# Optimization experiments

Hardware: AMD Instinct MI355X
Metric: run time of the kernel (lower is better)

The kernel has to match this reference:

```python
import jax, jax.numpy as jnp
import numpy as np

N_NODES = 32768
EMB_DIM = 128
N_CODES = 4096
N_GRAPHS = 512
ALPHA = 0.5            # args.alpha_init buffer
COMMIT_W = 1.0         # args.commitment_weight
BN_EPS = 1e-5


def setup_inputs() -> dict:
    key = jax.random.key(0)
    ks = jax.random.split(key, 8)
    node_feat = jax.random.normal(ks[0], (N_NODES, EMB_DIM), dtype=jnp.float32)
    score = jax.random.uniform(ks[1], (N_NODES, 1), dtype=jnp.float32)
    batch = jnp.sort(jax.random.randint(ks[2], (N_NODES,), 0, N_GRAPHS)).astype(jnp.int64)
    codebook_c = jax.random.normal(ks[3], (N_CODES, EMB_DIM), dtype=jnp.float32)
    codebook_s = jax.random.normal(ks[4], (N_CODES, EMB_DIM), dtype=jnp.float32)
    w1 = jax.random.normal(ks[5], (EMB_DIM, 2 * EMB_DIM), dtype=jnp.float32) * (1.0 / np.sqrt(EMB_DIM))
    b1 = jnp.zeros((2 * EMB_DIM,), dtype=jnp.float32)
    gamma = jnp.ones((2 * EMB_DIM,), dtype=jnp.float32)
    beta = jnp.zeros((2 * EMB_DIM,), dtype=jnp.float32)
    run_mean = jnp.zeros((2 * EMB_DIM,), dtype=jnp.float32)
    run_var = jnp.ones((2 * EMB_DIM,), dtype=jnp.float32)
    w2 = jax.random.normal(ks[6], (2 * EMB_DIM, 1), dtype=jnp.float32) * (1.0 / np.sqrt(2 * EMB_DIM))
    b2 = jnp.zeros((1,), dtype=jnp.float32)
    return {"node_feat": node_feat, "score": score, "batch": batch,
            "codebook_c": codebook_c, "codebook_s": codebook_s,
            "w1": w1, "b1": b1, "gamma": gamma, "beta": beta,
            "run_mean": run_mean, "run_var": run_var, "w2": w2, "b2": b2}


def _vector_quantize(x, codebook):
    # squared euclidean distance [N, K]; argmin lookup with straight-through.
    d2 = (jnp.sum(x * x, axis=-1, keepdims=True)
          - 2.0 * (x @ codebook.T)
          + jnp.sum(codebook * codebook, axis=-1))
    idx = jnp.argmin(d2, axis=-1)                     # [N]
    quantize = codebook[idx]                          # gather [N, D]
    commit_loss = jnp.mean((jax.lax.stop_gradient(quantize) - x) ** 2) * COMMIT_W
    out = x + jax.lax.stop_gradient(quantize - x)     # straight-through estimator
    return out, idx, commit_loss


def _mean_pool(x, batch):
    sums = jax.ops.segment_sum(x, batch, num_segments=N_GRAPHS)
    counts = jax.ops.segment_sum(jnp.ones((x.shape[0], 1), x.dtype), batch, num_segments=N_GRAPHS)
    return sums / jnp.maximum(counts, 1.0)


def reference(node_feat, score, batch, codebook_c, codebook_s,
              w1, b1, gamma, beta, run_mean, run_var, w2, b2):
    h_c = node_feat * score + ALPHA * node_feat * (1.0 - score)
    h_s = node_feat * (1.0 - score) + ALPHA * node_feat * score
    vq_c, _, cmt_loss_c = _vector_quantize(h_c, codebook_c)
    vq_s, _, cmt_loss_s = _vector_quantize(h_s, codebook_s)
    c_node_feat = node_feat * score + vq_c
    s_node_feat = node_feat * (1.0 - score) + vq_s
    c_graph_feat = _mean_pool(c_node_feat, batch)
    s_graph_feat = _mean_pool(s_node_feat, batch)
    # classifier: Linear -> BatchNorm1d (eval) -> ReLU -> Dropout(identity) -> Linear
    h = c_graph_feat @ w1 + b1
    h = (h - run_mean) * jax.lax.rsqrt(run_var + BN_EPS) * gamma + beta
    h = jax.nn.relu(h)
    c_logit = h @ w2 + b2
    return (c_logit, c_graph_feat, s_graph_feat, cmt_loss_c, cmt_loss_s, c_node_feat, s_node_feat)
```

## Files before the change

### kernel.cpp

```cpp
#include <hip/hip_runtime.h>
#include <hip/hip_bf16.h>

#define NODES   32768
#define DIM     128
#define NCODES  4096
#define NGRAPHS 512

#define OFF_LOGIT 0
#define OFF_CG    512
#define OFF_SG    66048
#define OFF_LC    131584
#define OFF_LS    131585
#define OFF_CN    131586
#define OFF_SN    4325890

#define SPLIT_U16   263680
#define PLANE_U16   524288
#define SLOT_F32    1180416

#define WS_CNORM    0
#define WS_IDX      32768
#define WS_LOSS     294912
#define WS_FLAGCNT  294928
#define WS_STARTS   294936
#define WS_FLAGLIST 296988
#define FLAG_CAP    32767

typedef __attribute__((ext_vector_type(8))) short bf16x8_t;
typedef __attribute__((ext_vector_type(4))) float f32x4_t;

__device__ __forceinline__ float h_of(float x, float sc, int cb) {
    float omsc = __fsub_rn(1.0f, sc);
    float half_x = __fmul_rn(0.5f, x);
    if (cb == 0)
        return __fadd_rn(__fmul_rn(x, sc), __fmul_rn(half_x, omsc));
    else
        return __fadd_rn(__fmul_rn(x, omsc), __fmul_rn(half_x, sc));
}

__device__ __forceinline__ unsigned short f2bf(float f) {
    __hip_bfloat16 b = __float2bfloat16(f);
    return *reinterpret_cast<unsigned short*>(&b);
}
__device__ __forceinline__ float bf2f(unsigned short u) {
    __hip_bfloat16 b = *reinterpret_cast<__hip_bfloat16*>(&u);
    return __bfloat162float(b);
}

__device__ __forceinline__ void gload_lds16(const void* g, void* l) {
    __builtin_amdgcn_global_load_lds(
        (const __attribute__((address_space(1))) int*)g,
        (__attribute__((address_space(3))) int*)l, 16, 0, 0);
}

__global__ __launch_bounds__(256) void prep_kernel(
    const float* __restrict__ cb_c, const float* __restrict__ cb_s,
    const int* __restrict__ batch,
    float* __restrict__ cnorm, unsigned short* __restrict__ splits,
    int* __restrict__ starts, int* __restrict__ flagcnt)
{
    int gwave = (blockIdx.x * 256 + threadIdx.x) >> 6;
    int lane  = threadIdx.x & 63;

    if (gwave < 2 * NCODES) {
        int cb = gwave >> 12, row = gwave & (NCODES - 1);
        const float* cp = (cb ? cb_s : cb_c) + (size_t)row * DIM;
        float2 v = ((const float2*)cp)[lane];
        float p = __fadd_rn(__fmul_rn(v.x, v.x), __fmul_rn(v.y, v.y));
        #pragma unroll
        for (int off = 32; off; off >>= 1) p = __fadd_rn(p, __shfl_xor(p, off, 64));
        if (lane == 0) cnorm[cb * NCODES + row] = p;
        unsigned short h0 = f2bf(v.x), h1 = f2bf(v.y);
        unsigned short l0 = f2bf(__fsub_rn(v.x, bf2f(h0)));
        unsigned short l1 = f2bf(__fsub_rn(v.y, bf2f(h1)));
        unsigned int* hp = (unsigned int*)(splits + (size_t)(cb * 2 + 0) * PLANE_U16);
        unsigned int* lp = (unsigned int*)(splits + (size_t)(cb * 2 + 1) * PLANE_U16);
        hp[row * 64 + lane] = (unsigned int)h0 | ((unsigned int)h1 << 16);
        lp[row * 64 + lane] = (unsigned int)l0 | ((unsigned int)l1 << 16);
    } else {
        int w1 = gwave - 2 * NCODES;
        int g = w1 * 64 + lane;
        if (g <= NGRAPHS) {
            int lo = 0, hi = NODES;
            while (lo < hi) { int mid = (lo + hi) >> 1; if (batch[mid] < g) lo = mid + 1; else hi = mid; }
            starts[g] = lo;
        }
        if (w1 == 0 && lane < 2) flagcnt[lane] = 0;
    }
}

__global__ __launch_bounds__(256, 2) void vq_main_kernel(
    const float* __restrict__ node_feat, const float* __restrict__ score,
    const unsigned short* __restrict__ splits, const float* __restrict__ cnorm,
    int* __restrict__ idx_ws, int* __restrict__ flagcnt, int* __restrict__ flaglist,
    unsigned long long* __restrict__ slots)
{
    __shared__ unsigned short lds[32768];
    const int cb    = blockIdx.y;
    const int nbase = blockIdx.x * 128;
    const int tid = threadIdx.x;
    const int w   = tid >> 6;
    const int l15 = tid & 15;
    const int lg  = (tid & 63) >> 4;
    const int swz = (tid & 7) << 4;
    const float* cnp = cnorm + cb * NCODES;

    if (tid < 128) slots[(size_t)cb * NODES + nbase + tid] = ~0ull;

    #pragma unroll
    for (int i = 0; i < 16; ++i) {
        int idx = i * 1024 + tid * 4;
        int row = idx >> 7, k = idx & 127;
        float4 x = *(const float4*)&node_feat[(size_t)(nbase + row) * DIM + k];
        float sc = score[nbase + row];
        float h0 = h_of(x.x, sc, cb), h1 = h_of(x.y, sc, cb);
        float h2 = h_of(x.z, sc, cb), h3 = h_of(x.w, sc, cb);
        unsigned short u0 = f2bf(h0), u1 = f2bf(h1), u2 = f2bf(h2), u3 = f2bf(h3);
        unsigned short v0 = f2bf(__fsub_rn(h0, bf2f(u0))), v1 = f2bf(__fsub_rn(h1, bf2f(u1)));
        unsigned short v2 = f2bf(__fsub_rn(h2, bf2f(u2))), v3 = f2bf(__fsub_rn(h3, bf2f(u3)));
        int abyte = row * 256 + ((2 * k) ^ ((row & 7) << 4));
        uint2 hw; hw.x = (unsigned)u0 | ((unsigned)u1 << 16); hw.y = (unsigned)u2 | ((unsigned)u3 << 16);
        uint2 lw; lw.x = (unsigned)v0 | ((unsigned)v1 << 16); lw.y = (unsigned)v2 | ((unsigned)v3 << 16);
        *(uint2*)((char*)lds + abyte) = hw;
        *(uint2*)((char*)lds + 32768 + abyte) = lw;
    }
    __syncthreads();

    bf16x8_t ahi[2][4], alo[2][4];
    int colbyte[4];
    #pragma unroll
    for (int ch = 0; ch < 4; ++ch) colbyte[ch] = (ch * 64 + lg * 16) ^ swz;
    #pragma unroll
    for (int rs = 0; rs < 2; ++rs)
        #pragma unroll
        for (int ch = 0; ch < 4; ++ch) {
            int row = 32 * w + 16 * rs + l15;
            int off = row * 256 + colbyte[ch];
            ahi[rs][ch] = *(const bf16x8_t*)((const char*)lds + off);
            alo[rs][ch] = *(const bf16x8_t*)((const char*)lds + 32768 + off);
        }
    __syncthreads();

    const unsigned short* wplane = splits + (size_t)(cb * 2 + (w >> 1)) * PLANE_U16;
    int soff[8];
    #pragma unroll
    for (int i = 0; i < 8; ++i) {
        int row = ((w & 1) << 5) + i * 4 + lg;
        soff[i] = row * 256 + ((l15 * 16) ^ ((row & 7) << 4));
    }

    {
        const char* tb = (const char*)wplane;
        #pragma unroll
        for (int i = 0; i < 8; ++i)
            gload_lds16(tb + soff[i], (char*)lds + w * 8192 + i * 1024);
    }
    float cnc[4], cnn[4];
    #pragma unroll
    for (int cs = 0; cs < 4; ++cs) cnc[cs] = cnp[cs * 16 + l15];
    __syncthreads();

    const float NEG_INF = -3.4e38f;
    float b1v[2][4], b2v[2][4]; int b1i[2][4];
    #pragma unroll
    for (int rs = 0; rs < 2; ++rs)
        #pragma unroll
        for (int r = 0; r < 4; ++r) { b1v[rs][r] = NEG_INF; b2v[rs][r] = NEG_INF; b1i[rs][r] = 0; }

    for (int t = 0; t < 64; ++t) {
        int bs_cur = (t & 1) << 15;
        if (t < 63) {
            int bs_nxt = ((t + 1) & 1) << 15;
            const char* tb = (const char*)wplane + (t + 1) * 16384;
            #pragma unroll
            for (int i = 0; i < 8; ++i)
                gload_lds16(tb + soff[i], (char*)lds + bs_nxt + w * 8192 + i * 1024);
            #pragma unroll
            for (int cs = 0; cs < 4; ++cs) cnn[cs] = cnp[(t + 1) * 64 + cs * 16 + l15];
        }

        f32x4_t acc[2][4];
        #pragma unroll
        for (int cs = 0; cs < 4; ++cs) {
            float iv = -0.5f * cnc[cs];
            f32x4_t ini = {iv, iv, iv, iv};
            acc[0][cs] = ini; acc[1][cs] = ini;
        }

        #pragma unroll
        for (int ch = 0; ch < 4; ++ch) {
            #pragma unroll
            for (int cs = 0; cs < 4; ++cs) {
                const char* bp = (const char*)lds + bs_cur + (cs * 16 + l15) * 256 + colbyte[ch];
                bf16x8_t bhi = *(const bf16x8_t*)bp;
                bf16x8_t blo = *(const bf16x8_t*)(bp + 16384);
                #pragma unroll
                for (int rs = 0; rs < 2; ++rs) {
                    acc[rs][cs] = __builtin_amdgcn_mfma_f32_16x16x32_bf16(ahi[rs][ch], bhi, acc[rs][cs], 0, 0, 0);
                    acc[rs][cs] = __builtin_amdgcn_mfma_f32_16x16x32_bf16(alo[rs][ch], bhi, acc[rs][cs], 0, 0, 0);
                    acc[rs][cs] = __builtin_amdgcn_mfma_f32_16x16x32_bf16(ahi[rs][ch], blo, acc[rs][cs], 0, 0, 0);
                }
            }
        }

        #pragma unroll
        for (int cs = 0; cs < 4; ++cs) {
            int code = t * 64 + cs * 16 + l15;
            #pragma unroll
            for (int rs = 0; rs < 2; ++rs)
                #pragma unroll
                for (int r = 0; r < 4; ++r) {
                    float a = acc[rs][cs][r];
                    bool gt = a > b1v[rs][r];
                    float nb2 = __builtin_amdgcn_fmed3f(a, b1v[rs][r], b2v[rs][r]);
                    if (gt) b1i[rs][r] = code;
                    b1v[rs][r] = fmaxf(a, b1v[rs][r]);
                    b2v[rs][r] = nb2;
                }
        }
        #pragma unroll
        for (int cs = 0; cs < 4; ++cs) cnc[cs] = cnn[cs];
        __syncthreads();
    }

    #pragma unroll
    for (int off = 1; off < 16; off <<= 1) {
        #pragma unroll
        for (int rs = 0; rs < 2; ++rs)
            #pragma unroll
            for (int r = 0; r < 4; ++r) {
                float ov1 = __shfl_xor(b1v[rs][r], off, 64);
                int   oi  = __shfl_xor(b1i[rs][r], off, 64);
                float ov2 = __shfl_xor(b2v[rs][r], off, 64);
                bool take = (ov1 > b1v[rs][r]) || (ov1 == b1v[rs][r] && oi < b1i[rs][r]);
                float loser = fminf(ov1, b1v[rs][r]);
                b1v[rs][r] = fmaxf(ov1, b1v[rs][r]);
                if (take) b1i[rs][r] = oi;
                b2v[rs][r] = fmaxf(loser, fmaxf(ov2, b2v[rs][r]));
            }
    }
    if (l15 == 0) {
        #pragma unroll
        for (int rs = 0; rs < 2; ++rs)
            #pragma unroll
            for (int r = 0; r < 4; ++r) {
                int node = nbase + 32 * w + 16 * rs + 4 * lg + r;
                idx_ws[cb * NODES + node] = b1i[rs][r];
                if (b1v[rs][r] - b2v[rs][r] < 0.04f) {
                    int p = atomicAdd(flagcnt + cb, 1);
                    if (p < FLAG_CAP) flaglist[cb * FLAG_CAP + p] = node;
                }
            }
    }
}

__global__ __launch_bounds__(256) void vq_cleanup_kernel(
    const float* __restrict__ node_feat, const float* __restrict__ score,
    const float* __restrict__ cb_c, const float* __restrict__ cb_s,
    const float* __restrict__ cnorm, const int* __restrict__ flagcnt,
    const int* __restrict__ flaglist, unsigned long long* __restrict__ slots)
{
    __shared__ float cbT[128][65];
    __shared__ float hbuf[4][128];
    const int cb  = blockIdx.y;
    const int seg = blockIdx.x & 63;
    const int ng  = blockIdx.x >> 6;
    const float* cbp = cb ? cb_s : cb_c;
    const int* list = flaglist + cb * FLAG_CAP;
    int cnt = flagcnt[cb]; if (cnt > FLAG_CAP) cnt = FLAG_CAP;
    const int tid = threadIdx.x, w = tid >> 6, l = tid & 63;

    {
        int c = tid >> 2, ks = (tid & 3) * 32;
        const float* src = cbp + (size_t)(seg * 64 + c) * DIM + ks;
        #pragma unroll
        for (int j = 0; j < 8; ++j) {
            float4 v = *(const float4*)(src + j * 4);
            cbT[ks + j * 4 + 0][c] = v.x;
            cbT[ks + j * 4 + 1][c] = v.y;
            cbT[ks + j * 4 + 2][c] = v.z;
            cbT[ks + j * 4 + 3][c] = v.w;
        }
    }
    const int mycode = seg * 64 + l;
    const float cn = cnorm[cb * NCODES + mycode];
    __syncthreads();

    for (int base = ng * 4; base < cnt; base += 32) {
        int e = base + w;
        bool valid = e < cnt;
        int node = list[valid ? e : 0];
        float sc = score[node];
        float x0 = node_feat[(size_t)node * DIM + l];
        float x1 = node_feat[(size_t)node * DIM + 64 + l];
        float h0 = h_of(x0, sc, cb), h1 = h_of(x1, sc, cb);
        hbuf[w][l] = h0; hbuf[w][64 + l] = h1;
        float sxx = __fadd_rn(__fmul_rn(h0, h0), __fmul_rn(h1, h1));
        #pragma unroll
        for (int off = 32; off; off >>= 1) sxx = __fadd_rn(sxx, __shfl_xor(sxx, off, 64));
        asm volatile("s_waitcnt lgkmcnt(0)" ::: "memory");

        float p0 = 0.f, p1 = 0.f, p2 = 0.f, p3 = 0.f;
        #pragma unroll 8
        for (int m = 0; m < 32; ++m) {
            p0 = fmaf(hbuf[w][4 * m + 0], cbT[4 * m + 0][l], p0);
            p1 = fmaf(hbuf[w][4 * m + 1], cbT[4 * m + 1][l], p1);
            p2 = fmaf(hbuf[w][4 * m + 2], cbT[4 * m + 2][l], p2);
            p3 = fmaf(hbuf[w][4 * m + 3], cbT[4 * m + 3][l], p3);
        }
        float dot = __fadd_rn(__fadd_rn(p0, p1), __fadd_rn(p2, p3));
        float d2 = __fadd_rn(__fsub_rn(sxx, __fmul_rn(2.0f, dot)), cn);

        unsigned b = __float_as_uint(d2);
        unsigned key = (b & 0x80000000u) ? ~b : (b | 0x80000000u);
        unsigned long long pk = ((unsigned long long)key << 32) | (unsigned)mycode;
        #pragma unroll
        for (int off = 1; off < 64; off <<= 1) {
            unsigned long long o = __shfl_xor(pk, off, 64);
            pk = (o < pk) ? o : pk;
        }
        if (valid && l == 0)
            atomicMin(&slots[(size_t)cb * NODES + node], pk);
        asm volatile("s_waitcnt lgkmcnt(0)" ::: "memory");
    }
}

__global__ __launch_bounds__(256) void flag_writeback_kernel(
    const int* __restrict__ flagcnt, const int* __restrict__ flaglist,
    const unsigned long long* __restrict__ slots, int* __restrict__ idx_ws)
{
    int gt = blockIdx.x * 256 + threadIdx.x;
    int c0 = flagcnt[0]; if (c0 > FLAG_CAP) c0 = FLAG_CAP;
    int c1 = flagcnt[1]; if (c1 > FLAG_CAP) c1 = FLAG_CAP;
    for (int e = gt; e < 2 * FLAG_CAP; e += 256 * 256) {
        int cb = (e >= FLAG_CAP) ? 1 : 0;
        int i = e - cb * FLAG_CAP;
        int cnt = cb ? c1 : c0;
        if (i < cnt) {
            int node = flaglist[cb * FLAG_CAP + i];
            idx_ws[cb * NODES + node] =
                (int)(slots[(size_t)cb * NODES + node] & 0xFFFFFFFFull);
        }
    }
}

__global__ __launch_bounds__(256) void gather_kernel(
    const float* __restrict__ node_feat, const float* __restrict__ score,
    const float* __restrict__ cb_c, const float* __restrict__ cb_s,
    const int* __restrict__ idx_all, float* __restrict__ out,
    double* __restrict__ partials)
{
    __shared__ float redc[4], reds[4];
    int wave = threadIdx.x >> 6, lane = threadIdx.x & 63;
    int node = blockIdx.x * 4 + wave;
    float sc = score[node];
    float2 x  = *(const float2*)&node_feat[(size_t)node * DIM + 2 * lane];
    int ic = idx_all[node], is_ = idx_all[NODES + node];
    float2 qc = *(const float2*)&cb_c[(size_t)ic * DIM + 2 * lane];
    float2 qs = *(const float2*)&cb_s[(size_t)is_ * DIM + 2 * lane];

    float omsc = __fsub_rn(1.0f, sc);
    float2 cn, sn;
    cn.x = __fadd_rn(__fmul_rn(x.x, sc), qc.x);
    cn.y = __fadd_rn(__fmul_rn(x.y, sc), qc.y);
    sn.x = __fadd_rn(__fmul_rn(x.x, omsc), qs.x);
    sn.y = __fadd_rn(__fmul_rn(x.y, omsc), qs.y);
    *(float2*)&out[OFF_CN + (size_t)node * DIM + 2 * lane] = cn;
    *(float2*)&out[OFF_SN + (size_t)node * DIM + 2 * lane] = sn;

    float hc1 = h_of(x.x, sc, 0), hc2 = h_of(x.y, sc, 0);
    float hs1 = h_of(x.x, sc, 1), hs2 = h_of(x.y, sc, 1);
    float d1 = qc.x - hc1, d2 = qc.y - hc2;
    float e1 = qs.x - hs1, e2 = qs.y - hs2;
    float lc = d1 * d1 + d2 * d2;
    float ls = e1 * e1 + e2 * e2;
    #pragma unroll
    for (int off = 32; off; off >>= 1) {
        lc += __shfl_down(lc, off, 64);
        ls += __shfl_down(ls, off, 64);
    }
    if (lane == 0) { redc[wave] = lc; reds[wave] = ls; }
    __syncthreads();
    if (threadIdx.x == 0) {
        double tc = (double)redc[0] + redc[1] + redc[2] + redc[3];
        double ts = (double)reds[0] + reds[1] + reds[2] + reds[3];
        partials[blockIdx.x] = tc;
        partials[8192 + blockIdx.x] = ts;
    }
}

__global__ __launch_bounds__(256) void loss_reduce_kernel(
    const double* __restrict__ partials, float* __restrict__ out)
{
    __shared__ double red[4];
    int b = blockIdx.x, t = threadIdx.x, w = t >> 6, l = t & 63;
    const double* p = partials + b * 8192;
    double s = 0.0;
    #pragma unroll 4
    for (int i = t; i < 8192; i += 256) s += p[i];
    #pragma unroll
    for (int off = 32; off; off >>= 1) s += __shfl_down(s, off, 64);
    if (l == 0) red[w] = s;
    __syncthreads();
    if (t == 0) {
        double tot = (red[0] + red[1]) + (red[2] + red[3]);
        out[OFF_LC + b] = (float)(tot * (1.0 / 4194304.0));
    }
}

__global__ __launch_bounds__(256) void pool_kernel(
    const int* __restrict__ starts, float* __restrict__ out)
{
    int g = blockIdx.x;
    int half = threadIdx.x >> 7, d = threadIdx.x & 127;
    int s = starts[g], e = starts[g + 1];
    const float* src = out + (half ? OFF_SN : OFF_CN);
    float sum = 0.0f;
    for (int n = s; n < e; ++n) sum = __fadd_rn(sum, src[(size_t)n * DIM + d]);
    float cnt = fmaxf((float)(e - s), 1.0f);
    out[(half ? OFF_SG : OFF_CG) + g * DIM + d] = __fdiv_rn(sum, cnt);
}

__global__ __launch_bounds__(256) void classifier_kernel(
    const float* __restrict__ w1, const float* __restrict__ b1,
    const float* __restrict__ gamma, const float* __restrict__ beta,
    const float* __restrict__ rm, const float* __restrict__ rv,
    const float* __restrict__ w2, const float* __restrict__ b2,
    float* __restrict__ out)
{
    __shared__ float row[DIM];
    __shared__ float red[4];
    int g = blockIdx.x, t = threadIdx.x;
    if (t < DIM) row[t] = out[OFF_CG + g * DIM + t];
    __syncthreads();
    float h = 0.0f;
    #pragma unroll 8
    for (int k = 0; k < DIM; ++k) h = fmaf(row[k], w1[k * 256 + t], h);
    h = __fadd_rn(h, b1[t]);
    float inv = __frsqrt_rn(__fadd_rn(rv[t], 1e-5f));
    h = __fadd_rn(__fmul_rn(__fmul_rn(__fsub_rn(h, rm[t]), inv), gamma[t]), beta[t]);
    h = fmaxf(h, 0.0f);
    float p = __fmul_rn(h, w2[t]);
    #pragma unroll
    for (int off = 32; off; off >>= 1) p += __shfl_down(p, off, 64);
    if ((t & 63) == 0) red[t >> 6] = p;
    __syncthreads();
    if (t == 0) {
        float total = __fadd_rn(__fadd_rn(red[0], red[1]), __fadd_rn(red[2], red[3]));
        out[OFF_LOGIT + g] = __fadd_rn(total, b2[0]);
    }
}

extern "C" void kernel_launch(void* const* d_in, const int* in_sizes, int n_in,
                              void* d_out, int out_size, void* d_ws, size_t ws_size,
                              hipStream_t stream) {
    const float* node_feat = (const float*)d_in[0];
    const float* score     = (const float*)d_in[1];
    const int*   batch     = (const int*)d_in[2];
    const float* cb_c      = (const float*)d_in[3];
    const float* cb_s      = (const float*)d_in[4];
    const float* w1        = (const float*)d_in[5];
    const float* b1        = (const float*)d_in[6];
    const float* gamma     = (const float*)d_in[7];
    const float* beta      = (const float*)d_in[8];
    const float* rm        = (const float*)d_in[9];
    const float* rv        = (const float*)d_in[10];
    const float* w2        = (const float*)d_in[11];
    const float* b2        = (const float*)d_in[12];
    float* out = (float*)d_out;
    char*  ws  = (char*)d_ws;

    float*  cnorm    = (float*)(ws + WS_CNORM);
    int*    idx      = (int*)(ws + WS_IDX);
    int*    flagcnt  = (int*)(ws + WS_FLAGCNT);
    int*    starts   = (int*)(ws + WS_STARTS);
    int*    flaglist = (int*)(ws + WS_FLAGLIST);
    unsigned short* splits = (unsigned short*)d_out + SPLIT_U16;
    unsigned long long* slots = (unsigned long long*)(out + SLOT_F32);
    double* partials = (double*)(out + OFF_CG);

    prep_kernel<<<2051, 256, 0, stream>>>(cb_c, cb_s, batch, cnorm, splits,
                                          starts, flagcnt);
    vq_main_kernel<<<dim3(256, 2), 256, 0, stream>>>(node_feat, score, splits, cnorm,
                                                     idx, flagcnt, flaglist, slots);
    vq_cleanup_kernel<<<dim3(512, 2), 256, 0, stream>>>(node_feat, score, cb_c, cb_s,
                                                        cnorm, flagcnt, flaglist, slots);
    flag_writeback_kernel<<<256, 256, 0, stream>>>(flagcnt, flaglist, slots, idx);
    gather_kernel<<<8192, 256, 0, stream>>>(node_feat, score, cb_c, cb_s, idx, out, partials);
    loss_reduce_kernel<<<2, 256, 0, stream>>>(partials, out);
    pool_kernel<<<512, 256, 0, stream>>>(starts, out);
    classifier_kernel<<<512, 256, 0, stream>>>(w1, b1, gamma, beta, rm, rv, w2, b2, out);
}
```

Before: 384.3 us.

## Use single fp16 MFMA pass with split codebook halves and resolve kernel

Replaces the three-pass bf16 hi/lo split distance GEMM with one fp16 MFMA pass, which removes two thirds of the matrix work and the low-precision planes. The codebook search is split across two blocks per node tile so that twice as many blocks run with smaller LDS and higher occupancy. A new resolve kernel merges the two half results and builds the ambiguity flag list with a wave-aggregated atomic. The flag threshold is widened to absorb the larger fp16 error, which sends more nodes to the exact fp32 cleanup pass; the cleanup grid is doubled to handle them.

```diff
diff --git a/kernel.cpp b/kernel.cpp
--- a/kernel.cpp
+++ b/kernel.cpp
@@ -5,6 +5,7 @@
 #define DIM     128
 #define NCODES  4096
 #define NGRAPHS 512
+#define THR     0.0625f
 
 #define OFF_LOGIT 0
 #define OFF_CG    512
@@ -16,17 +17,17 @@
 
 #define SPLIT_U16   263680
 #define PLANE_U16   524288
-#define SLOT_F32    1180416
+#define HALF_F32    1180416
+#define CSLOT_F32   1442560
 
 #define WS_CNORM    0
 #define WS_IDX      32768
-#define WS_LOSS     294912
 #define WS_FLAGCNT  294928
 #define WS_STARTS   294936
 #define WS_FLAGLIST 296988
 #define FLAG_CAP    32767
 
-typedef __attribute__((ext_vector_type(8))) short bf16x8_t;
+typedef __attribute__((ext_vector_type(8))) _Float16 f16x8_t;
 typedef __attribute__((ext_vector_type(4))) float f32x4_t;
 
 __device__ __forceinline__ float h_of(float x, float sc, int cb) {
@@ -38,19 +39,23 @@
         return __fadd_rn(__fmul_rn(x, omsc), __fmul_rn(half_x, sc));
 }
 
-__device__ __forceinline__ unsigned short f2bf(float f) {
-    __hip_bfloat16 b = __float2bfloat16(f);
-    return *reinterpret_cast<unsigned short*>(&b);
-}
-__device__ __forceinline__ float bf2f(unsigned short u) {
-    __hip_bfloat16 b = *reinterpret_cast<__hip_bfloat16*>(&u);
-    return __bfloat162float(b);
+__device__ __forceinline__ unsigned short f2h(float f) {
+    return __builtin_bit_cast(unsigned short, (_Float16)f);
 }
 
 __device__ __forceinline__ void gload_lds16(const void* g, void* l) {
     __builtin_amdgcn_global_load_lds(
         (const __attribute__((address_space(1))) int*)g,
         (__attribute__((address_space(3))) int*)l, 16, 0, 0);
+}
+
+__device__ __forceinline__ unsigned sortkey(float f) {
+    unsigned b = __float_as_uint(f);
+    return (b & 0x80000000u) ? ~b : (b | 0x80000000u);
+}
+__device__ __forceinline__ float keyinv(unsigned k) {
+    unsigned b = (k & 0x80000000u) ? (k & 0x7FFFFFFFu) : ~k;
+    return __uint_as_float(b);
 }
 
 __global__ __launch_bounds__(256) void prep_kernel(
@@ -70,13 +75,8 @@
         #pragma unroll
         for (int off = 32; off; off >>= 1) p = __fadd_rn(p, __shfl_xor(p, off, 64));
         if (lane == 0) cnorm[cb * NCODES + row] = p;
-        unsigned short h0 = f2bf(v.x), h1 = f2bf(v.y);
-        unsigned short l0 = f2bf(__fsub_rn(v.x, bf2f(h0)));
-        unsigned short l1 = f2bf(__fsub_rn(v.y, bf2f(h1)));
-        unsigned int* hp = (unsigned int*)(splits + (size_t)(cb * 2 + 0) * PLANE_U16);
-        unsigned int* lp = (unsigned int*)(splits + (size_t)(cb * 2 + 1) * PLANE_U16);
-        hp[row * 64 + lane] = (unsigned int)h0 | ((unsigned int)h1 << 16);
-        lp[row * 64 + lane] = (unsigned int)l0 | ((unsigned int)l1 << 16);
+        unsigned int* hp = (unsigned int*)(splits + (size_t)cb * PLANE_U16);
+        hp[row * 64 + lane] = (unsigned)f2h(v.x) | ((unsigned)f2h(v.y) << 16);
     } else {
         int w1 = gwave - 2 * NCODES;
         int g = w1 * 64 + lane;
@@ -89,23 +89,22 @@
     }
 }
 
-__global__ __launch_bounds__(256, 2) void vq_main_kernel(
+__global__ __launch_bounds__(256, 4) void vq_main_kernel(
     const float* __restrict__ node_feat, const float* __restrict__ score,
     const unsigned short* __restrict__ splits, const float* __restrict__ cnorm,
-    int* __restrict__ idx_ws, int* __restrict__ flagcnt, int* __restrict__ flaglist,
-    unsigned long long* __restrict__ slots)
-{
-    __shared__ unsigned short lds[32768];
+    unsigned long long* __restrict__ halfres)
+{
+    __shared__ unsigned short lds[16384];
+    const int nb    = blockIdx.x & 255;
+    const int half  = blockIdx.x >> 8;
     const int cb    = blockIdx.y;
-    const int nbase = blockIdx.x * 128;
+    const int nbase = nb * 128;
     const int tid = threadIdx.x;
     const int w   = tid >> 6;
     const int l15 = tid & 15;
     const int lg  = (tid & 63) >> 4;
     const int swz = (tid & 7) << 4;
-    const float* cnp = cnorm + cb * NCODES;
-
-    if (tid < 128) slots[(size_t)cb * NODES + nbase + tid] = ~0ull;
+    const float* cnp = cnorm + cb * NCODES + half * 2048;
 
     #pragma unroll
     for (int i = 0; i < 16; ++i) {
@@ -113,20 +112,15 @@
         int row = idx >> 7, k = idx & 127;
         float4 x = *(const float4*)&node_feat[(size_t)(nbase + row) * DIM + k];
         float sc = score[nbase + row];
-        float h0 = h_of(x.x, sc, cb), h1 = h_of(x.y, sc, cb);
-        float h2 = h_of(x.z, sc, cb), h3 = h_of(x.w, sc, cb);
-        unsigned short u0 = f2bf(h0), u1 = f2bf(h1), u2 = f2bf(h2), u3 = f2bf(h3);
-        unsigned short v0 = f2bf(__fsub_rn(h0, bf2f(u0))), v1 = f2bf(__fsub_rn(h1, bf2f(u1)));
-        unsigned short v2 = f2bf(__fsub_rn(h2, bf2f(u2))), v3 = f2bf(__fsub_rn(h3, bf2f(u3)));
+        unsigned u0 = f2h(h_of(x.x, sc, cb)), u1 = f2h(h_of(x.y, sc, cb));
+        unsigned u2 = f2h(h_of(x.z, sc, cb)), u3 = f2h(h_of(x.w, sc, cb));
         int abyte = row * 256 + ((2 * k) ^ ((row & 7) << 4));
-        uint2 hw; hw.x = (unsigned)u0 | ((unsigned)u1 << 16); hw.y = (unsigned)u2 | ((unsigned)u3 << 16);
-        uint2 lw; lw.x = (unsigned)v0 | ((unsigned)v1 << 16); lw.y = (unsigned)v2 | ((unsigned)v3 << 16);
+        uint2 hw; hw.x = u0 | (u1 << 16); hw.y = u2 | (u3 << 16);
         *(uint2*)((char*)lds + abyte) = hw;
-        *(uint2*)((char*)lds + 32768 + abyte) = lw;
-    }
-    __syncthreads();
-
-    bf16x8_t ahi[2][4], alo[2][4];
+    }
+    __syncthreads();
+
+    f16x8_t ahi[2][4];
     int colbyte[4];
     #pragma unroll
     for (int ch = 0; ch < 4; ++ch) colbyte[ch] = (ch * 64 + lg * 16) ^ swz;
@@ -135,29 +129,24 @@
         #pragma unroll
         for (int ch = 0; ch < 4; ++ch) {
             int row = 32 * w + 16 * rs + l15;
-            int off = row * 256 + colbyte[ch];
-            ahi[rs][ch] = *(const bf16x8_t*)((const char*)lds + off);
-            alo[rs][ch] = *(const bf16x8_t*)((const char*)lds + 32768 + off);
-        }
-    __syncthreads();
-
-    const unsigned short* wplane = splits + (size_t)(cb * 2 + (w >> 1)) * PLANE_U16;
-    int soff[8];
-    #pragma unroll
-    for (int i = 0; i < 8; ++i) {
-        int row = ((w & 1) << 5) + i * 4 + lg;
+            ahi[rs][ch] = *(const f16x8_t*)((const char*)lds + row * 256 + colbyte[ch]);
+        }
+    __syncthreads();
+
+    const unsigned short* wplane = splits + (size_t)cb * PLANE_U16 + half * 262144;
+    int soff[4];
+    #pragma unroll
+    for (int i = 0; i < 4; ++i) {
+        int row = w * 16 + i * 4 + lg;
         soff[i] = row * 256 + ((l15 * 16) ^ ((row & 7) << 4));
     }
 
     {
         const char* tb = (const char*)wplane;
         #pragma unroll
-        for (int i = 0; i < 8; ++i)
-            gload_lds16(tb + soff[i], (char*)lds + w * 8192 + i * 1024);
-    }
-    float cnc[4], cnn[4];
-    #pragma unroll
-    for (int cs = 0; cs < 4; ++cs) cnc[cs] = cnp[cs * 16 + l15];
+        for (int i = 0; i < 4; ++i)
+            gload_lds16(tb + soff[i], (char*)lds + w * 4096 + i * 1024);
+    }
     __syncthreads();
 
     const float NEG_INF = -3.4e38f;
@@ -167,59 +156,55 @@
         #pragma unroll
         for (int r = 0; r < 4; ++r) { b1v[rs][r] = NEG_INF; b2v[rs][r] = NEG_INF; b1i[rs][r] = 0; }
 
-    for (int t = 0; t < 64; ++t) {
-        int bs_cur = (t & 1) << 15;
-        if (t < 63) {
-            int bs_nxt = ((t + 1) & 1) << 15;
+    for (int t = 0; t < 32; ++t) {
+        int bs_cur = (t & 1) << 14;
+        float cnc[4];
+        #pragma unroll
+        for (int cs = 0; cs < 4; ++cs) cnc[cs] = cnp[t * 64 + cs * 16 + l15];
+        if (t < 31) {
+            int bs_nxt = ((t + 1) & 1) << 14;
             const char* tb = (const char*)wplane + (t + 1) * 16384;
             #pragma unroll
-            for (int i = 0; i < 8; ++i)
-                gload_lds16(tb + soff[i], (char*)lds + bs_nxt + w * 8192 + i * 1024);
-            #pragma unroll
-            for (int cs = 0; cs < 4; ++cs) cnn[cs] = cnp[(t + 1) * 64 + cs * 16 + l15];
-        }
-
-        f32x4_t acc[2][4];
-        #pragma unroll
-        for (int cs = 0; cs < 4; ++cs) {
-            float iv = -0.5f * cnc[cs];
-            f32x4_t ini = {iv, iv, iv, iv};
-            acc[0][cs] = ini; acc[1][cs] = ini;
-        }
-
-        #pragma unroll
-        for (int ch = 0; ch < 4; ++ch) {
-            #pragma unroll
-            for (int cs = 0; cs < 4; ++cs) {
-                const char* bp = (const char*)lds + bs_cur + (cs * 16 + l15) * 256 + colbyte[ch];
-                bf16x8_t bhi = *(const bf16x8_t*)bp;
-                bf16x8_t blo = *(const bf16x8_t*)(bp + 16384);
-                #pragma unroll
-                for (int rs = 0; rs < 2; ++rs) {
-                    acc[rs][cs] = __builtin_amdgcn_mfma_f32_16x16x32_bf16(ahi[rs][ch], bhi, acc[rs][cs], 0, 0, 0);
-                    acc[rs][cs] = __builtin_amdgcn_mfma_f32_16x16x32_bf16(alo[rs][ch], bhi, acc[rs][cs], 0, 0, 0);
-                    acc[rs][cs] = __builtin_amdgcn_mfma_f32_16x16x32_bf16(ahi[rs][ch], blo, acc[rs][cs], 0, 0, 0);
-                }
-            }
-        }
-
-        #pragma unroll
-        for (int cs = 0; cs < 4; ++cs) {
-            int code = t * 64 + cs * 16 + l15;
+            for (int i = 0; i < 4; ++i)
+                gload_lds16(tb + soff[i], (char*)lds + bs_nxt + w * 4096 + i * 1024);
+        }
+
+        #pragma unroll
+        for (int cp = 0; cp < 2; ++cp) {
+            f32x4_t acc[2][2];
             #pragma unroll
             for (int rs = 0; rs < 2; ++rs)
                 #pragma unroll
-                for (int r = 0; r < 4; ++r) {
-                    float a = acc[rs][cs][r];
-                    bool gt = a > b1v[rs][r];
-                    float nb2 = __builtin_amdgcn_fmed3f(a, b1v[rs][r], b2v[rs][r]);
-                    if (gt) b1i[rs][r] = code;
-                    b1v[rs][r] = fmaxf(a, b1v[rs][r]);
-                    b2v[rs][r] = nb2;
+                for (int c2 = 0; c2 < 2; ++c2) acc[rs][c2] = (f32x4_t){0.f, 0.f, 0.f, 0.f};
+
+            #pragma unroll
+            for (int ch = 0; ch < 4; ++ch)
+                #pragma unroll
+                for (int c2 = 0; c2 < 2; ++c2) {
+                    int cs = cp * 2 + c2;
+                    f16x8_t bh = *(const f16x8_t*)((const char*)lds + bs_cur +
+                                                   (cs * 16 + l15) * 256 + colbyte[ch]);
+                    acc[0][c2] = __builtin_amdgcn_mfma_f32_16x16x32_f16(ahi[0][ch], bh, acc[0][c2], 0, 0, 0);
+                    acc[1][c2] = __builtin_amdgcn_mfma_f32_16x16x32_f16(ahi[1][ch], bh, acc[1][c2], 0, 0, 0);
                 }
-        }
-        #pragma unroll
-        for (int cs = 0; cs < 4; ++cs) cnc[cs] = cnn[cs];
+
+            #pragma unroll
+            for (int c2 = 0; c2 < 2; ++c2) {
+                int cs = cp * 2 + c2;
+                int code = half * 2048 + t * 64 + cs * 16 + l15;
+                #pragma unroll
+                for (int rs = 0; rs < 2; ++rs)
+                    #pragma unroll
+                    for (int r = 0; r < 4; ++r) {
+                        float a = __fmaf_rn(-0.5f, cnc[cs], acc[rs][c2][r]);
+                        bool gt = a > b1v[rs][r];
+                        float nb2 = __builtin_amdgcn_fmed3f(a, b1v[rs][r], b2v[rs][r]);
+                        if (gt) b1i[rs][r] = code;
+                        b1v[rs][r] = fmaxf(a, b1v[rs][r]);
+                        b2v[rs][r] = nb2;
+                    }
+            }
+        }
         __syncthreads();
     }
 
@@ -245,12 +230,43 @@
             #pragma unroll
             for (int r = 0; r < 4; ++r) {
                 int node = nbase + 32 * w + 16 * rs + 4 * lg + r;
-                idx_ws[cb * NODES + node] = b1i[rs][r];
-                if (b1v[rs][r] - b2v[rs][r] < 0.04f) {
-                    int p = atomicAdd(flagcnt + cb, 1);
-                    if (p < FLAG_CAP) flaglist[cb * FLAG_CAP + p] = node;
-                }
+                unsigned key = sortkey(b1v[rs][r]);
+                unsigned pay = (unsigned)b1i[rs][r] |
+                               ((b1v[rs][r] - b2v[rs][r] < THR) ? 0x1000u : 0u);
+                halfres[((size_t)(cb * 2 + half)) * NODES + node] =
+                    ((unsigned long long)key << 32) | pay;
             }
+    }
+}
+
+__global__ __launch_bounds__(256) void resolve_kernel(
+    const unsigned long long* __restrict__ hr, unsigned long long* __restrict__ cslot,
+    int* __restrict__ idx_ws, int* __restrict__ flagcnt, int* __restrict__ flaglist)
+{
+    int cb = blockIdx.y;
+    int node = blockIdx.x * 256 + threadIdx.x;
+    unsigned long long A = hr[((size_t)(cb * 2 + 0)) * NODES + node];
+    unsigned long long B = hr[((size_t)(cb * 2 + 1)) * NODES + node];
+    unsigned ka = (unsigned)(A >> 32), kb = (unsigned)(B >> 32);
+    bool awin = ka >= kb;
+    unsigned long long W = awin ? A : B;
+    float aw = keyinv(awin ? ka : kb);
+    float al = keyinv(awin ? kb : ka);
+    bool flag = ((W >> 12) & 1ull) || (__fsub_rn(aw, al) < THR);
+    idx_ws[cb * NODES + node] = (int)(W & 0xFFFu);
+    if (flag) cslot[(size_t)cb * NODES + node] = ~0ull;
+
+    unsigned long long mask = __ballot(flag);
+    if (mask) {
+        int lane = threadIdx.x & 63;
+        int leader = __ffsll((long long)mask) - 1;
+        int base = 0;
+        if (lane == leader) base = atomicAdd(flagcnt + cb, (int)__popcll(mask));
+        base = __shfl(base, leader, 64);
+        if (flag) {
+            int pos = base + (int)__popcll(mask & ((1ull << lane) - 1ull));
+            if (pos < FLAG_CAP) flaglist[cb * FLAG_CAP + pos] = node;
+        }
     }
 }
 
@@ -286,7 +302,7 @@
     const float cn = cnorm[cb * NCODES + mycode];
     __syncthreads();
 
-    for (int base = ng * 4; base < cnt; base += 32) {
+    for (int base = ng * 4; base < cnt; base += 64) {
         int e = base + w;
         bool valid = e < cnt;
         int node = list[valid ? e : 0];
@@ -382,10 +398,8 @@
     if (lane == 0) { redc[wave] = lc; reds[wave] = ls; }
     __syncthreads();
     if (threadIdx.x == 0) {
-        double tc = (double)redc[0] + redc[1] + redc[2] + redc[3];
-        double ts = (double)reds[0] + reds[1] + reds[2] + reds[3];
-        partials[blockIdx.x] = tc;
-        partials[8192 + blockIdx.x] = ts;
+        partials[blockIdx.x]        = (double)redc[0] + redc[1] + redc[2] + redc[3];
+        partials[8192 + blockIdx.x] = (double)reds[0] + reds[1] + reds[2] + reds[3];
     }
 }
 
@@ -476,16 +490,19 @@
     int*    starts   = (int*)(ws + WS_STARTS);
     int*    flaglist = (int*)(ws + WS_FLAGLIST);
     unsigned short* splits = (unsigned short*)d_out + SPLIT_U16;
-    unsigned long long* slots = (unsigned long long*)(out + SLOT_F32);
+    unsigned long long* halfres = (unsigned long long*)(out + HALF_F32);
+    unsigned long long* cslot   = (unsigned long long*)(out + CSLOT_F32);
     double* partials = (double*)(out + OFF_CG);
 
     prep_kernel<<<2051, 256, 0, stream>>>(cb_c, cb_s, batch, cnorm, splits,
                                           starts, flagcnt);
-    vq_main_kernel<<<dim3(256, 2), 256, 0, stream>>>(node_feat, score, splits, cnorm,
-                                                     idx, flagcnt, flaglist, slots);
-    vq_cleanup_kernel<<<dim3(512, 2), 256, 0, stream>>>(node_feat, score, cb_c, cb_s,
-                                                        cnorm, flagcnt, flaglist, slots);
-    flag_writeback_kernel<<<256, 256, 0, stream>>>(flagcnt, flaglist, slots, idx);
+    vq_main_kernel<<<dim3(512, 2), 256, 0, stream>>>(node_feat, score, splits, cnorm,
+                                                     halfres);
+    resolve_kernel<<<dim3(128, 2), 256, 0, stream>>>(halfres, cslot, idx,
+                                                     flagcnt, flaglist);
+    vq_cleanup_kernel<<<dim3(1024, 2), 256, 0, stream>>>(node_feat, score, cb_c, cb_s,
+                                                         cnorm, flagcnt, flaglist, cslot);
+    flag_writeback_kernel<<<256, 256, 0, stream>>>(flagcnt, flaglist, cslot, idx);
     gather_kernel<<<8192, 256, 0, stream>>>(node_feat, score, cb_c, cb_s, idx, out, partials);
     loss_reduce_kernel<<<2, 256, 0, stream>>>(partials, out);
     pool_kernel<<<512, 256, 0, stream>>>(starts, out);
```

Result: faster. 350.3 us (-8.8%).
